# Kernel tuning notes

Hardware: AMD Instinct MI355X
Metric: run time of the kernel (lower is better)

The kernel has to match this reference:

```python
import jax, jax.numpy as jnp
import numpy as np

N, K, D = 131072, 512, 512
ALPHA = 1.0


def setup_inputs() -> dict:
    key = jax.random.key(0)
    kx, kc = jax.random.split(key)
    x = jax.random.normal(kx, (N, D), dtype=jnp.float32)
    # Xavier uniform for clusters: limit = sqrt(6/(K+D))
    limit = float(np.sqrt(6.0 / (K + D)))
    clusters = jax.random.uniform(kc, (K, D), dtype=jnp.float32, minval=-limit, maxval=limit)
    return {"x": x, "clusters": clusters}


def reference(x, clusters):
    # mathematically equal to sum((x[:,None,:]-c[None,:,:])**2, axis=2)
    x2 = jnp.sum(x * x, axis=1, keepdims=True)            # (N, 1)
    c2 = jnp.sum(clusters * clusters, axis=1)             # (K,)
    d2 = x2 + c2[None, :] - 2.0 * (x @ clusters.T)        # (N, K)
    d2 = jnp.maximum(d2, 0.0)  # guard tiny negatives from cancellation
    q = 1.0 / (1.0 + d2 / ALPHA)
    q = q ** ((ALPHA + 1.0) / 2.0)
    q = q / jnp.sum(q, axis=1, keepdims=True)
    return q
```

## Files before the change

kernel.cpp:

```cpp
#include <hip/hip_runtime.h>
#include <hip/hip_bf16.h>
#include <stdint.h>

#define N_ROWS 131072
#define K_CL   512
#define D_DIM  512
#define M_TILE 128
#define BK     32
#define STEPS  (D_DIM / BK)

typedef __attribute__((ext_vector_type(8))) short short8;
typedef __attribute__((ext_vector_type(4))) float f32x4;

__device__ __forceinline__ unsigned short f2bf(float f) {
  union { float f; unsigned u; } v; v.f = f;
  unsigned r = v.u + 0x7fffu + ((v.u >> 16) & 1u);
  return (unsigned short)(r >> 16);
}

__global__ void prep_c2(const float* __restrict__ c, float* __restrict__ c2) {
  const int b = blockIdx.x;
  const int l = threadIdx.x;
  const float* row = c + (size_t)b * D_DIM;
  float s = 0.f;
  #pragma unroll
  for (int i = 0; i < 2; ++i) {
    const int col = i * 256 + l * 4;
    float4 v = *(const float4*)(row + col);
    s += v.x * v.x + v.y * v.y + v.z * v.z + v.w * v.w;
  }
  #pragma unroll
  for (int m = 1; m < 64; m <<= 1) s += __shfl_xor(s, m);
  if (l == 0) c2[b] = s;
}

__global__ void pack_b(const float* __restrict__ c, unsigned short* __restrict__ pb) {
  const int bid = blockIdx.x;
  const int c16 = bid & 31;
  const int kk  = bid >> 5;
  const int l   = threadIdx.x;
  const int row = c16 * 16 + (l & 15);
  const int k0  = kk * 32 + (l >> 4) * 8;
  float4 v0 = *(const float4*)(c + (size_t)row * D_DIM + k0);
  float4 v1 = *(const float4*)(c + (size_t)row * D_DIM + k0 + 4);
  ushort4 u0 = make_ushort4(f2bf(v0.x), f2bf(v0.y), f2bf(v0.z), f2bf(v0.w));
  ushort4 u1 = make_ushort4(f2bf(v1.x), f2bf(v1.y), f2bf(v1.z), f2bf(v1.w));
  *(ushort4*)(pb + (size_t)(bid * 64 + l) * 8)     = u0;
  *(ushort4*)(pb + (size_t)(bid * 64 + l) * 8 + 4) = u1;
}

__global__ __launch_bounds__(512, 2)
void cluster_main(const float* __restrict__ x,
                  const unsigned short* __restrict__ pb,
                  const float* __restrict__ c2,
                  float* __restrict__ out) {
  __shared__ short As[2][M_TILE * 40];
  __shared__ float c2s[K_CL];
  __shared__ float x2s[M_TILE];
  __shared__ float rowsum[4][M_TILE];
  __shared__ float rinv[M_TILE];

  const int t = threadIdx.x;
  const int w  = t >> 6;
  const int wr = w >> 2;
  const int wc = w & 3;
  const int l = t & 63;
  const int row0 = blockIdx.x * M_TILE;

  c2s[t] = c2[t];

  f32x4 acc[4][8];
  #pragma unroll
  for (int i = 0; i < 4; ++i)
    #pragma unroll
    for (int j = 0; j < 8; ++j) acc[i][j] = (f32x4){0.f, 0.f, 0.f, 0.f};

  const int rowA = t >> 3;
  const int rowB = rowA + 64;
  const int kc   = (t & 7) * 4;
  float ssA = 0.f, ssB = 0.f;

  const float* xA = x + (size_t)(row0 + rowA) * D_DIM + kc;
  const float* xB = x + (size_t)(row0 + rowB) * D_DIM + kc;

  float4 va = *(const float4*)(xA);
  float4 vb = *(const float4*)(xB);

  int cur = 0;
  for (int kk = 0; kk < STEPS; ++kk) {
    ssA += va.x * va.x + va.y * va.y + va.z * va.z + va.w * va.w;
    ssB += vb.x * vb.x + vb.y * vb.y + vb.z * vb.z + vb.w * vb.w;
    *(ushort4*)&As[cur][rowA * 40 + kc] =
        make_ushort4(f2bf(va.x), f2bf(va.y), f2bf(va.z), f2bf(va.w));
    *(ushort4*)&As[cur][rowB * 40 + kc] =
        make_ushort4(f2bf(vb.x), f2bf(vb.y), f2bf(vb.z), f2bf(vb.w));

    if (kk + 1 < STEPS) {
      va = *(const float4*)(xA + (kk + 1) * BK);
      vb = *(const float4*)(xB + (kk + 1) * BK);
    }

    const unsigned short* pbk = pb + ((size_t)(kk * 32 + wc * 8) * 64 + l) * 8;
    short8 b[8];
    #pragma unroll
    for (int ct = 0; ct < 8; ++ct)
      b[ct] = *(const short8*)(pbk + (size_t)ct * 64 * 8);

    __syncthreads();

    short8 a[4];
    #pragma unroll
    for (int rt = 0; rt < 4; ++rt)
      a[rt] = *(const short8*)&As[cur][(wr * 64 + rt * 16 + (l & 15)) * 40 + (l >> 4) * 8];

    #pragma unroll
    for (int ct = 0; ct < 8; ++ct)
      #pragma unroll
      for (int rt = 0; rt < 4; ++rt)
        acc[rt][ct] = __builtin_amdgcn_mfma_f32_16x16x32_bf16(a[rt], b[ct], acc[rt][ct], 0, 0, 0);

    cur ^= 1;
  }

  float s1 = ssA, s2 = ssB;
  s1 += __shfl_xor(s1, 1); s1 += __shfl_xor(s1, 2); s1 += __shfl_xor(s1, 4);
  s2 += __shfl_xor(s2, 1); s2 += __shfl_xor(s2, 2); s2 += __shfl_xor(s2, 4);
  if ((t & 7) == 0) { x2s[rowA] = s1; x2s[rowB] = s2; }
  __syncthreads();

  const int lg = l >> 4;
  const int ln = l & 15;

  float xr[4][4];
  #pragma unroll
  for (int rt = 0; rt < 4; ++rt)
    #pragma unroll
    for (int r = 0; r < 4; ++r) xr[rt][r] = x2s[wr * 64 + rt * 16 + lg * 4 + r];
  float cv[8];
  #pragma unroll
  for (int ct = 0; ct < 8; ++ct) cv[ct] = c2s[wc * 128 + ct * 16 + ln];

  float rp[4][4];
  #pragma unroll
  for (int rt = 0; rt < 4; ++rt)
    #pragma unroll
    for (int r = 0; r < 4; ++r) rp[rt][r] = 0.f;

  #pragma unroll
  for (int rt = 0; rt < 4; ++rt)
    #pragma unroll
    for (int ct = 0; ct < 8; ++ct) {
      f32x4 s = acc[rt][ct], q;
      #pragma unroll
      for (int r = 0; r < 4; ++r) {
        float d2 = xr[rt][r] + cv[ct] - 2.f * s[r];
        d2 = fmaxf(d2, 0.f);
        float qq = __builtin_amdgcn_rcpf(1.f + d2);
        q[r] = qq;
        rp[rt][r] += qq;
      }
      acc[rt][ct] = q;
    }

  #pragma unroll
  for (int m = 1; m < 16; m <<= 1)
    #pragma unroll
    for (int rt = 0; rt < 4; ++rt)
      #pragma unroll
      for (int r = 0; r < 4; ++r) rp[rt][r] += __shfl_xor(rp[rt][r], m);

  if (ln == 0)
    #pragma unroll
    for (int rt = 0; rt < 4; ++rt)
      #pragma unroll
      for (int r = 0; r < 4; ++r)
        rowsum[wc][wr * 64 + rt * 16 + lg * 4 + r] = rp[rt][r];
  __syncthreads();

  if (t < M_TILE) {
    float tot = rowsum[0][t] + rowsum[1][t] + rowsum[2][t] + rowsum[3][t];
    rinv[t] = __builtin_amdgcn_rcpf(tot);
  }
  __syncthreads();

  float ri[4][4];
  #pragma unroll
  for (int rt = 0; rt < 4; ++rt)
    #pragma unroll
    for (int r = 0; r < 4; ++r) ri[rt][r] = rinv[wr * 64 + rt * 16 + lg * 4 + r];

  #pragma unroll
  for (int rt = 0; rt < 4; ++rt)
    #pragma unroll
    for (int ct = 0; ct < 8; ++ct)
      #pragma unroll
      for (int r = 0; r < 4; ++r)
        __builtin_nontemporal_store(
            acc[rt][ct][r] * ri[rt][r],
            &out[(size_t)(row0 + wr * 64 + rt * 16 + lg * 4 + r) * K_CL + wc * 128 + ct * 16 + ln]);
}

extern "C" void kernel_launch(void* const* d_in, const int* in_sizes, int n_in,
                              void* d_out, int out_size, void* d_ws, size_t ws_size,
                              hipStream_t stream) {
  const float* x        = (const float*)d_in[0];
  const float* clusters = (const float*)d_in[1];
  float* out = (float*)d_out;

  unsigned short* pbuf = (unsigned short*)d_ws;
  float* c2 = (float*)((char*)d_ws + (size_t)K_CL * D_DIM * sizeof(unsigned short));

  prep_c2<<<K_CL, 64, 0, stream>>>(clusters, c2);
  pack_b<<<STEPS * 32, 64, 0, stream>>>(clusters, pbuf);
  cluster_main<<<N_ROWS / M_TILE, 512, 0, stream>>>(x, pbuf, c2, out);
}
```

Before: 496.9 us.

## Deepen x prefetch, split B loads around MFMAs, use lightweight LDS barrier

The K loop is unrolled by two with two register sets for x, so global loads of x are issued two steps ahead. The packed-B loads are split into two halves, with the second half interleaved after the first 16 MFMAs. __syncthreads is replaced by an explicit lgkmcnt(0) wait plus s_barrier, so outstanding global prefetches no longer stall at the barrier. The aim is to hide global-memory latency behind MFMA work, at the cost of more live registers in an already register-heavy kernel.

```diff
diff --git a/kernel.cpp b/kernel.cpp
--- a/kernel.cpp
+++ b/kernel.cpp
@@ -49,6 +49,44 @@
   *(ushort4*)(pb + (size_t)(bid * 64 + l) * 8 + 4) = u1;
 }
 
+#define MF4(CT, B)                                                              \
+  acc[0][CT] = __builtin_amdgcn_mfma_f32_16x16x32_bf16(a0, B, acc[0][CT], 0, 0, 0); \
+  acc[1][CT] = __builtin_amdgcn_mfma_f32_16x16x32_bf16(a1, B, acc[1][CT], 0, 0, 0); \
+  acc[2][CT] = __builtin_amdgcn_mfma_f32_16x16x32_bf16(a2, B, acc[2][CT], 0, 0, 0); \
+  acc[3][CT] = __builtin_amdgcn_mfma_f32_16x16x32_bf16(a3, B, acc[3][CT], 0, 0, 0);
+
+#define KBODY(KS, VA, VB, PF)                                                   \
+  {                                                                             \
+    ssA += VA.x * VA.x + VA.y * VA.y + VA.z * VA.z + VA.w * VA.w;               \
+    ssB += VB.x * VB.x + VB.y * VB.y + VB.z * VB.z + VB.w * VB.w;               \
+    *(ushort4*)&As[cur][rowA * 40 + kc] =                                       \
+        make_ushort4(f2bf(VA.x), f2bf(VA.y), f2bf(VA.z), f2bf(VA.w));           \
+    *(ushort4*)&As[cur][rowB * 40 + kc] =                                       \
+        make_ushort4(f2bf(VB.x), f2bf(VB.y), f2bf(VB.z), f2bf(VB.w));           \
+    const unsigned short* pbk = pb + ((size_t)((KS) * 32 + wc * 8) * 64 + l) * 8; \
+    short8 b0 = *(const short8*)(pbk + 0 * 512);                                \
+    short8 b1 = *(const short8*)(pbk + 1 * 512);                                \
+    short8 b2 = *(const short8*)(pbk + 2 * 512);                                \
+    short8 b3 = *(const short8*)(pbk + 3 * 512);                                \
+    asm volatile("s_waitcnt lgkmcnt(0)" ::: "memory");                          \
+    __builtin_amdgcn_s_barrier();                                               \
+    short8 a0 = *(const short8*)&As[cur][(wr * 64 +  0 + ln) * 40 + lg * 8];    \
+    short8 a1 = *(const short8*)&As[cur][(wr * 64 + 16 + ln) * 40 + lg * 8];    \
+    short8 a2 = *(const short8*)&As[cur][(wr * 64 + 32 + ln) * 40 + lg * 8];    \
+    short8 a3 = *(const short8*)&As[cur][(wr * 64 + 48 + ln) * 40 + lg * 8];    \
+    MF4(0, b0) MF4(1, b1) MF4(2, b2) MF4(3, b3)                                 \
+    short8 b4 = *(const short8*)(pbk + 4 * 512);                                \
+    short8 b5 = *(const short8*)(pbk + 5 * 512);                                \
+    short8 b6 = *(const short8*)(pbk + 6 * 512);                                \
+    short8 b7 = *(const short8*)(pbk + 7 * 512);                                \
+    if (PF) {                                                                   \
+      VA = *(const float4*)(xA + ((KS) + 2) * BK);                              \
+      VB = *(const float4*)(xB + ((KS) + 2) * BK);                              \
+    }                                                                           \
+    MF4(4, b4) MF4(5, b5) MF4(6, b6) MF4(7, b7)                                 \
+    cur ^= 1;                                                                   \
+  }
+
 __global__ __launch_bounds__(512, 2)
 void cluster_main(const float* __restrict__ x,
                   const unsigned short* __restrict__ pb,
@@ -65,6 +103,8 @@
   const int wr = w >> 2;
   const int wc = w & 3;
   const int l = t & 63;
+  const int lg = l >> 4;
+  const int ln = l & 15;
   const int row0 = blockIdx.x * M_TILE;
 
   c2s[t] = c2[t];
@@ -83,53 +123,24 @@
   const float* xA = x + (size_t)(row0 + rowA) * D_DIM + kc;
   const float* xB = x + (size_t)(row0 + rowB) * D_DIM + kc;
 
-  float4 va = *(const float4*)(xA);
-  float4 vb = *(const float4*)(xB);
+  float4 va0 = *(const float4*)(xA);
+  float4 vb0 = *(const float4*)(xB);
+  float4 va1 = *(const float4*)(xA + BK);
+  float4 vb1 = *(const float4*)(xB + BK);
 
   int cur = 0;
-  for (int kk = 0; kk < STEPS; ++kk) {
-    ssA += va.x * va.x + va.y * va.y + va.z * va.z + va.w * va.w;
-    ssB += vb.x * vb.x + vb.y * vb.y + vb.z * vb.z + vb.w * vb.w;
-    *(ushort4*)&As[cur][rowA * 40 + kc] =
-        make_ushort4(f2bf(va.x), f2bf(va.y), f2bf(va.z), f2bf(va.w));
-    *(ushort4*)&As[cur][rowB * 40 + kc] =
-        make_ushort4(f2bf(vb.x), f2bf(vb.y), f2bf(vb.z), f2bf(vb.w));
-
-    if (kk + 1 < STEPS) {
-      va = *(const float4*)(xA + (kk + 1) * BK);
-      vb = *(const float4*)(xB + (kk + 1) * BK);
-    }
-
-    const unsigned short* pbk = pb + ((size_t)(kk * 32 + wc * 8) * 64 + l) * 8;
-    short8 b[8];
-    #pragma unroll
-    for (int ct = 0; ct < 8; ++ct)
-      b[ct] = *(const short8*)(pbk + (size_t)ct * 64 * 8);
-
-    __syncthreads();
-
-    short8 a[4];
-    #pragma unroll
-    for (int rt = 0; rt < 4; ++rt)
-      a[rt] = *(const short8*)&As[cur][(wr * 64 + rt * 16 + (l & 15)) * 40 + (l >> 4) * 8];
-
-    #pragma unroll
-    for (int ct = 0; ct < 8; ++ct)
-      #pragma unroll
-      for (int rt = 0; rt < 4; ++rt)
-        acc[rt][ct] = __builtin_amdgcn_mfma_f32_16x16x32_bf16(a[rt], b[ct], acc[rt][ct], 0, 0, 0);
-
-    cur ^= 1;
-  }
+  for (int k2 = 0; k2 < STEPS - 2; k2 += 2) {
+    KBODY(k2,     va0, vb0, true)
+    KBODY(k2 + 1, va1, vb1, true)
+  }
+  KBODY(STEPS - 2, va0, vb0, false)
+  KBODY(STEPS - 1, va1, vb1, false)
 
   float s1 = ssA, s2 = ssB;
   s1 += __shfl_xor(s1, 1); s1 += __shfl_xor(s1, 2); s1 += __shfl_xor(s1, 4);
   s2 += __shfl_xor(s2, 1); s2 += __shfl_xor(s2, 2); s2 += __shfl_xor(s2, 4);
   if ((t & 7) == 0) { x2s[rowA] = s1; x2s[rowB] = s2; }
   __syncthreads();
-
-  const int lg = l >> 4;
-  const int ln = l & 15;
 
   float xr[4][4];
   #pragma unroll
```

New measurement: 505.4 us. About the same (+1.7%).
